# Kernel tuning notes

Measured on AMD Instinct MI355X. Metric: run time of the kernel, lower is better.

Reference implementation:

```python
import jax, jax.numpy as jnp
import numpy as np

N, D_PHY, D_BOND, VOC = 512, 4, 128, 1024


def setup_inputs() -> dict:
    rng = np.random.default_rng(0)

    def cplx(shape, scale=1.0):
        return ((rng.standard_normal(shape) + 1j * rng.standard_normal(shape)) * scale).astype(np.complex64)

    A = cplx((VOC, D_PHY, D_PHY))                      # raw embedding params (QR applied in forward, as in torch M property)
    B0 = cplx((D_PHY, 1, D_BOND), 1.0 / np.sqrt(D_BOND))
    Bm = cplx((N - 2, D_PHY * D_BOND, D_BOND))
    Bm = np.linalg.qr(Bm)[0].reshape(N - 2, D_PHY, D_BOND, D_BOND).astype(np.complex64)  # left-isometric, as set_left_param
    Bl = cplx((D_PHY * D_BOND, 1))
    Bl = np.linalg.qr(Bl)[0].reshape(D_PHY, D_BOND, 1).astype(np.complex64)
    tokens = rng.integers(0, VOC, size=(N,))
    return {
        'a_re': jnp.asarray(A.real), 'a_im': jnp.asarray(A.imag),
        'b0_re': jnp.asarray(B0.real), 'b0_im': jnp.asarray(B0.imag),
        'bm_re': jnp.asarray(Bm.real), 'bm_im': jnp.asarray(Bm.imag),
        'bl_re': jnp.asarray(Bl.real), 'bl_im': jnp.asarray(Bl.imag),
        'tokens': jnp.asarray(tokens, dtype=jnp.int32),
    }


def _site(S, B, Mi):
    # S: (l, l') running density-like state; B: (p, l, r); Mi: (p, q) measurement op.
    # Equivalent to contracting torch's zipped = einsum(conj(B)[p,l,r], M[p,q], B[q,l',r'] -> [l,r,r',l'])
    # with the running state, but fused to avoid the (l,r,r',l') intermediate.
    t = jnp.einsum('ab,qbc->qac', S, B)      # (q, l, r')
    t = jnp.einsum('pq,qac->pac', Mi, t)     # (p, l, r')
    return jnp.einsum('plr,plc->rc', B.conj(), t)  # (r, r')


def reference(a_re, a_im, b0_re, b0_im, bm_re, bm_im, bl_re, bl_im, tokens):
    A = a_re + 1j * a_im                                  # (v, d, d)
    d = A.shape[-1]
    Aq = jnp.linalg.qr(A.reshape(-1, d))[0].reshape(A.shape)
    M = jnp.einsum('vij,vik->vjk', Aq.conj(), Aq)         # (v, d, d) POVM-like ops
    Ms = M[tokens]                                        # (n, d, d)

    B0 = b0_re + 1j * b0_im                               # (d, 1, D)
    Bm = bm_re + 1j * bm_im                               # (n-2, d, D, D)
    Bl = bl_re + 1j * bl_im                               # (d, D, 1)

    S = jnp.ones((1, 1), dtype=A.dtype)
    S = _site(S, B0, Ms[0])                               # (D, D)

    def step(S, xs):
        B, Mi = xs
        return _site(S, B, Mi), None

    S, _ = jax.lax.scan(step, S, (Bm, Ms[1:-1]))
    S = _site(S, Bl, Ms[-1])                              # (1, 1)
    return S.reshape(-1)                                  # complex64, shape (1,), as torch out.view(-1)
```

## Files before the change

kernel.cpp:

```cpp
#include <hip/hip_runtime.h>
#include <hip/hip_bf16.h>


__device__ __forceinline__ float2 cfma(float2 a, float2 b, float2 acc) {
    acc.x = fmaf(a.x, b.x, fmaf(-a.y, b.y, acc.x));
    acc.y = fmaf(a.x, b.y, fmaf( a.y, b.x, acc.y));
    return acc;
}
__device__ __forceinline__ float2 cfmac(float2 a, float2 b, float2 acc) {
    acc.x = fmaf(a.x, b.x, fmaf( a.y, b.y, acc.x));
    acc.y = fmaf(a.x, b.y, fmaf(-a.y, b.x, acc.y));
    return acc;
}

__device__ __forceinline__ float2 ld_coh(const float2* p) {
    union { unsigned long long u; float2 f; } cv;
    cv.u = __hip_atomic_load((const unsigned long long*)p,
                             __ATOMIC_RELAXED, __HIP_MEMORY_SCOPE_AGENT);
    return cv.f;
}
__device__ __forceinline__ void st_coh(float2* p, float2 x) {
    union { unsigned long long u; float2 f; } cv;
    cv.f = x;
    __hip_atomic_store((unsigned long long*)p, cv.u,
                       __ATOMIC_RELAXED, __HIP_MEMORY_SCOPE_AGENT);
}

__device__ __forceinline__ double2 d2mul(double2 a, double2 b) {
    return make_double2(a.x*b.x - a.y*b.y, a.x*b.y + a.y*b.x);
}
__device__ __forceinline__ double2 d2conj(double2 a) { return make_double2(a.x, -a.y); }
__device__ __forceinline__ double2 d2add(double2 a, double2 b) {
    return make_double2(a.x + b.x, a.y + b.y);
}
__device__ __forceinline__ double2 d2sub(double2 a, double2 b) {
    return make_double2(a.x - b.x, a.y - b.y);
}

__device__ __forceinline__ void lds_barrier() {
    asm volatile("s_waitcnt lgkmcnt(0)" ::: "memory");
    __builtin_amdgcn_s_barrier();
    __builtin_amdgcn_sched_barrier(0);
}

__device__ void redN(double2* v, int n, double2 (*redm)[4]) {
    for (int off = 32; off; off >>= 1) {
        for (int d = 0; d < n; ++d) {
            v[d].x += __shfl_down(v[d].x, off, 64);
            v[d].y += __shfl_down(v[d].y, off, 64);
        }
    }
    const int wid = threadIdx.x >> 6, lane = threadIdx.x & 63;
    __syncthreads();
    if (lane == 0)
        for (int d = 0; d < n; ++d) redm[wid][d] = v[d];
    __syncthreads();
    for (int d = 0; d < n; ++d) {
        double2 s = make_double2(0.0, 0.0);
        for (int w = 0; w < 9; ++w) { s.x += redm[w][d].x; s.y += redm[w][d].y; }
        v[d] = s;
    }
}

__device__ __forceinline__ float2 m_entry(const float* __restrict__ a_re,
                                          const float* __restrict__ a_im,
                                          int v, int m, const float2* Wl)
{
    const int j = m >> 2, k = m & 3;
    float2 Arow[4][4];
    #pragma unroll
    for (int i = 0; i < 4; ++i) {
        float4 re = *(const float4*)(a_re + v*16 + i*4);
        float4 im = *(const float4*)(a_im + v*16 + i*4);
        Arow[i][0] = make_float2(re.x, im.x);
        Arow[i][1] = make_float2(re.y, im.y);
        Arow[i][2] = make_float2(re.z, im.z);
        Arow[i][3] = make_float2(re.w, im.w);
    }
    float2 acc = make_float2(0.f, 0.f);
    #pragma unroll
    for (int i = 0; i < 4; ++i) {
        float2 yj = make_float2(0.f, 0.f), yk = yj;
        #pragma unroll
        for (int q = 0; q < 4; ++q) {
            yj = cfma(Arow[i][q], Wl[q*4 + j], yj);
            yk = cfma(Arow[i][q], Wl[q*4 + k], yk);
        }
        acc = cfmac(yj, yk, acc);
    }
    return acc;
}

__global__ __launch_bounds__(512) void zero_cnt(unsigned int* __restrict__ cnt)
{
    cnt[threadIdx.x] = 0u;
}

#define NWG 128u
__device__ __forceinline__ bool site_barrier(unsigned int* addr,
                                             unsigned* nzw, int* live_lds, int tid)
{
    asm volatile("s_waitcnt lgkmcnt(0)" ::: "memory");
    if (tid < 128) asm volatile("s_waitcnt vmcnt(0)" ::: "memory");
    __builtin_amdgcn_s_barrier();
    __builtin_amdgcn_sched_barrier(0);
    if (tid == 0) {
        unsigned add = 1u | ((nzw[0] | nzw[1]) ? 0x10000u : 0u);
        __hip_atomic_fetch_add(addr, add, __ATOMIC_RELAXED, __HIP_MEMORY_SCOPE_AGENT);
        unsigned v;
        for (;;) {
            v = __hip_atomic_load(addr, __ATOMIC_RELAXED, __HIP_MEMORY_SCOPE_AGENT);
            if ((v & 0xffffu) >= NWG) break;
            __builtin_amdgcn_s_sleep(1);
        }
        *live_lds = (int)(v >> 16);
    }
    asm volatile("s_waitcnt lgkmcnt(0)" ::: "memory");
    __builtin_amdgcn_s_barrier();
    __builtin_amdgcn_sched_barrier(0);
    return *live_lds != 0;
}

__global__ __launch_bounds__(576, 3) void scan_kernel(
    const float* __restrict__ a_re,  const float* __restrict__ a_im,
    const float* __restrict__ b0_re, const float* __restrict__ b0_im,
    const float* __restrict__ bm_re, const float* __restrict__ bm_im,
    const float* __restrict__ bl_re, const float* __restrict__ bl_im,
    const int*  __restrict__ tokens,
    float2* SbufA, float2* SbufB,
    unsigned int* cnt, float* out, int out_size)
{
    const int tid = threadIdx.x;
    const int bid = blockIdx.x;
    const int c   = ((bid & 7) << 4) | (bid >> 3);
    const int i16 = bid >> 3;

    __shared__ float2 Clds[4][128];
    __shared__ float4 Upart4[8][256];
    __shared__ float4 U4[256];
    __shared__ float4 P16_4[16][64];
    __shared__ float2 Bpre[2][4][128];
    __shared__ float2 fred[16];
    __shared__ double2 redm[9][4];
    __shared__ float2 Wlds[16];
    __shared__ float2 MtLds[2][16];
    __shared__ unsigned nzw[2];
    __shared__ int live_lds;

    const int a = tid & 127;
    const int h = tid >> 7;

    float2* Sread = SbufA;
    float2* Swrite = SbufB;
    bool dead = false;
    float warmacc = 0.f;
    float wm0 = 0.f, wm1 = 0.f, wm2 = 0.f, wm3 = 0.f;

    if (tid < 512) {
        const float4* t0r = (const float4*)bm_re + i16*1024;
        const float4* t0i = (const float4*)bm_im + i16*1024;
        #pragma unroll
        for (int k = 0; k < 2; ++k) {
            float4 x0 = t0r[tid + k*512],          y0 = t0i[tid + k*512];
            float4 x1 = t0r[16384 + tid + k*512],  y1 = t0i[16384 + tid + k*512];
            warmacc += x0.x+x0.y+x0.z+x0.w + y0.x+y0.y+y0.z+y0.w
                     + x1.x+x1.y+x1.z+x1.w + y1.x+y1.y+y1.z+y1.w;
        }
    }

    double2 gp[10];
    #pragma unroll
    for (int e = 0; e < 10; ++e) gp[e] = make_double2(0.0, 0.0);
    if (tid < 512) {
        for (int rr = 0; rr < 8; ++rr) {
            const int r = tid * 8 + rr;
            float4 fre = *(const float4*)(a_re + r*4);
            float4 fim = *(const float4*)(a_im + r*4);
            double r0 = fre.x, r1 = fre.y, r2 = fre.z, r3 = fre.w;
            double i0 = fim.x, i1 = fim.y, i2 = fim.z, i3 = fim.w;
#define GACC(e, rj, ij, rk, ik) \
            gp[e].x += rj*rk + ij*ik; gp[e].y += rj*ik - ij*rk;
            GACC(0, r0, i0, r0, i0)  GACC(1, r0, i0, r1, i1)
            GACC(2, r0, i0, r2, i2)  GACC(3, r0, i0, r3, i3)
            GACC(4, r1, i1, r1, i1)  GACC(5, r1, i1, r2, i2)
            GACC(6, r1, i1, r3, i3)  GACC(7, r2, i2, r2, i2)
            GACC(8, r2, i2, r3, i3)  GACC(9, r3, i3, r3, i3)
#undef GACC
        }
    }
    redN(gp + 0, 4, redm);
    redN(gp + 4, 4, redm);
    redN(gp + 8, 2, redm);

    double2 G4[4][4];
    G4[0][0]=gp[0]; G4[0][1]=gp[1]; G4[0][2]=gp[2]; G4[0][3]=gp[3];
    G4[1][1]=gp[4]; G4[1][2]=gp[5]; G4[1][3]=gp[6];
    G4[2][2]=gp[7]; G4[2][3]=gp[8]; G4[3][3]=gp[9];
    G4[1][0]=d2conj(gp[1]); G4[2][0]=d2conj(gp[2]); G4[3][0]=d2conj(gp[3]);
    G4[2][1]=d2conj(gp[5]); G4[3][1]=d2conj(gp[6]); G4[3][2]=d2conj(gp[8]);
    G4[0][0].y=0.0; G4[1][1].y=0.0; G4[2][2].y=0.0; G4[3][3].y=0.0;

    {
        double2 T[4][4];
        #pragma unroll
        for (int i = 0; i < 4; ++i)
            #pragma unroll
            for (int j = 0; j < 4; ++j)
                T[i][j] = make_double2((double)a_re[i*4+j], (double)a_im[i*4+j]);

        double dsgn[4];
        #pragma unroll
        for (int k = 0; k < 4; ++k) {
            double ssum = 0.0;
            #pragma unroll
            for (int i = 0; i < 4; ++i)
                if (i <= k) ssum += T[i][k].x*T[i][k].x + T[i][k].y*T[i][k].y;
            double xn = G4[k][k].x - ssum; if (xn < 0.0) xn = 0.0;
            double ar = T[k][k].x, ai = T[k][k].y;
            double nrm = sqrt(ar*ar + ai*ai + xn);
            double beta = (ar >= 0.0) ? -nrm : nrm;
            dsgn[k] = (beta >= 0.0) ? 1.0 : -1.0;
            double2 tau = make_double2((beta - ar)/beta, -ai/beta);
            double dr = ar - beta, di = ai;
            double dd = dr*dr + di*di;
            double2 s = make_double2(dr/dd, -di/dd);
            double2 w[4];
            #pragma unroll
            for (int j = 0; j < 4; ++j) if (j > k) {
                double2 acc = G4[k][j];
                #pragma unroll
                for (int i = 0; i < 4; ++i)
                    if (i <= k) acc = d2sub(acc, d2mul(d2conj(T[i][k]), T[i][j]));
                w[j] = d2add(T[k][j], d2mul(d2conj(s), acc));
            }
            #pragma unroll
            for (int j = 0; j < 4; ++j) if (j > k) {
                double2 tw = d2mul(tau, w[j]);
                T[k][j] = d2sub(T[k][j], tw);
                #pragma unroll
                for (int i = 0; i < 4; ++i)
                    if (i > k) T[i][j] = d2sub(T[i][j], d2mul(tw, d2mul(s, T[i][k])));
            }
            T[k][k] = make_double2(beta, 0.0);
            #pragma unroll
            for (int i = 0; i < 4; ++i)
                if (i > k) T[i][k] = make_double2(0.0, 0.0);
        }

        double2 R[4][4];
        #pragma unroll
        for (int k = 0; k < 4; ++k) {
            double dk = G4[k][k].x;
            #pragma unroll
            for (int i = 0; i < 4; ++i)
                if (i < k) dk -= R[i][k].x*R[i][k].x + R[i][k].y*R[i][k].y;
            if (dk < 1e-30) dk = 1e-30;
            double rkk = sqrt(dk);
            R[k][k] = make_double2(rkk, 0.0);
            #pragma unroll
            for (int j = 0; j < 4; ++j) if (j > k) {
                double2 acc = G4[k][j];
                #pragma unroll
                for (int i = 0; i < 4; ++i)
                    if (i < k) acc = d2sub(acc, d2mul(d2conj(R[i][k]), R[i][j]));
                R[k][j] = make_double2(acc.x/rkk, acc.y/rkk);
            }
        }
        double2 X[4][4];
        #pragma unroll
        for (int j = 0; j < 4; ++j) {
            #pragma unroll
            for (int i = 0; i < 4; ++i) X[i][j] = make_double2(0.0, 0.0);
            X[j][j] = make_double2(1.0 / R[j][j].x, 0.0);
            #pragma unroll
            for (int ii = 0; ii < 3; ++ii) {
                const int i = j - 1 - ii;
                if (i >= 0) {
                    double2 acc = make_double2(0.0, 0.0);
                    #pragma unroll
                    for (int m2 = 0; m2 < 4; ++m2)
                        if (m2 > i && m2 <= j) acc = d2add(acc, d2mul(R[i][m2], X[m2][j]));
                    X[i][j] = make_double2(-acc.x / R[i][i].x, -acc.y / R[i][i].x);
                }
            }
        }
        if (tid == 0) {
            #pragma unroll
            for (int q = 0; q < 4; ++q)
                #pragma unroll
                for (int j = 0; j < 4; ++j)
                    Wlds[q*4 + j] = make_float2((float)(X[q][j].x * dsgn[j]),
                                                (float)(X[q][j].y * dsgn[j]));
        }
    }
    __syncthreads();

    if (tid < 32) {
        const int which = tid >> 4, m = tid & 15;
        MtLds[which][m] = m_entry(a_re, a_im, tokens[which], m, Wlds);
    }
    if (tid < 512) {
        Bpre[1][h][a] = make_float2(bm_re[(h*128 + a)*128 + c],
                                    bm_im[(h*128 + a)*128 + c]);
    }
    __syncthreads();

    if (tid < 128) {
        const int r = a;
        float2 brr[4], bcc[4];
        for (int p = 0; p < 4; ++p) {
            brr[p] = make_float2(b0_re[p*128 + r], b0_im[p*128 + r]);
            bcc[p] = make_float2(b0_re[p*128 + c], b0_im[p*128 + c]);
        }
        float2 acc = make_float2(0.f, 0.f);
        for (int p = 0; p < 4; ++p) {
            float2 tp = make_float2(0.f, 0.f);
            for (int q = 0; q < 4; ++q) tp = cfma(MtLds[0][p*4 + q], bcc[q], tp);
            acc = cfmac(brr[p], tp, acc);
        }
        st_coh(&SbufA[c*128 + r], acc);
        int nz = (acc.x != 0.f) || (acc.y != 0.f);
        unsigned long long m = __ballot(nz);
        if ((tid & 63) == 0) nzw[tid >> 6] = (m != 0ULL) ? 1u : 0u;
    }

    if (!site_barrier(&cnt[0], nzw, &live_lds, tid)) dead = true;

    if (!dead) {
        for (int t = 1; t <= 510; ++t) {
            const int cur = t & 1, nxt = cur ^ 1;
            const float* br = bm_re + (size_t)(t - 1) * 65536;
            const float* bi = bm_im + (size_t)(t - 1) * 65536;

            float2 bp[8];
            float2 macc = make_float2(0.f, 0.f);
            int j = 0;
            if (tid >= 512) {
                j = tid - 512;
                warmacc += wm0 + wm1 + wm2 + wm3;
                if (t < 510) {
                    const float* br2 = bm_re + (size_t)t * 65536;
                    const float* bi2 = bm_im + (size_t)t * 65536;
                    #pragma unroll
                    for (int e = 0; e < 8; ++e) {
                        const int idx = j + e*64, q = idx >> 7, a2i = idx & 127;
                        bp[e] = make_float2(br2[(q*128 + a2i)*128 + c],
                                            bi2[(q*128 + a2i)*128 + c]);
                    }
                }
                if (j < 16) macc = m_entry(a_re, a_im, tokens[t+1], j, Wlds);
                if (t < 509) {
                    const float* wr = bm_re + (size_t)(t+1)*65536 + i16*4096;
                    const float* wi = bm_im + (size_t)(t+1)*65536 + i16*4096;
                    wm0 = wr[j*32];  wm1 = wr[2048 + j*32];
                    wm2 = wi[j*32];  wm3 = wi[2048 + j*32];
                } else { wm0 = wm1 = wm2 = wm3 = 0.f; }
            }

            if (tid < 512) {
                float2 acc = make_float2(0.f, 0.f);
                #pragma unroll
                for (int q = 0; q < 4; ++q)
                    acc = cfma(MtLds[cur][h*4 + q], Bpre[cur][q][a], acc);
                Clds[h][a] = acc;
            }
            lds_barrier();

            if (tid < 512) {
                const int sub = tid >> 6, a2 = tid & 63;
                float2 u00 = make_float2(0,0), u01 = u00, u02 = u00, u03 = u00;
                float2 u10 = u00, u11 = u00, u12 = u00, u13 = u00;
                {
                    const float2* _b0 = Sread + (sub*16)*128 + 2*a2;
                    const float2* _b1 = _b0 + 512;
                    const float2* _b2 = _b0 + 1024;
                    const float2* _b3 = _b0 + 1536;
                    float4 t0,t1,t2,t3,t4,t5,t6,t7,t8,t9,t10,t11,t12,t13,t14,t15;
                    asm volatile(
                      "global_load_dwordx4 %0, %16, off sc0 sc1\n\t"
                      "global_load_dwordx4 %1, %16, off offset:1024 sc0 sc1\n\t"
                      "global_load_dwordx4 %2, %16, off offset:2048 sc0 sc1\n\t"
                      "global_load_dwordx4 %3, %16, off offset:3072 sc0 sc1\n\t"
                      "global_load_dwordx4 %4, %17, off sc0 sc1\n\t"
                      "global_load_dwordx4 %5, %17, off offset:1024 sc0 sc1\n\t"
                      "global_load_dwordx4 %6, %17, off offset:2048 sc0 sc1\n\t"
                      "global_load_dwordx4 %7, %17, off offset:3072 sc0 sc1\n\t"
                      "global_load_dwordx4 %8, %18, off sc0 sc1\n\t"
                      "global_load_dwordx4 %9, %18, off offset:1024 sc0 sc1\n\t"
                      "global_load_dwordx4 %10, %18, off offset:2048 sc0 sc1\n\t"
                      "global_load_dwordx4 %11, %18, off offset:3072 sc0 sc1\n\t"
                      "global_load_dwordx4 %12, %19, off sc0 sc1\n\t"
                      "global_load_dwordx4 %13, %19, off offset:1024 sc0 sc1\n\t"
                      "global_load_dwordx4 %14, %19, off offset:2048 sc0 sc1\n\t"
                      "global_load_dwordx4 %15, %19, off offset:3072 sc0 sc1\n\t"
                      "s_waitcnt vmcnt(0)"
                      : "=&v"(t0), "=&v"(t1), "=&v"(t2), "=&v"(t3),
                        "=&v"(t4), "=&v"(t5), "=&v"(t6), "=&v"(t7),
                        "=&v"(t8), "=&v"(t9), "=&v"(t10), "=&v"(t11),
                        "=&v"(t12), "=&v"(t13), "=&v"(t14), "=&v"(t15)
                      : "v"(_b0), "v"(_b1), "v"(_b2), "v"(_b3));
                    float4 tt[16] = {t0,t1,t2,t3,t4,t5,t6,t7,
                                     t8,t9,t10,t11,t12,t13,t14,t15};
                    #pragma unroll
                    for (int e = 0; e < 16; ++e) {
                        const int b = sub*16 + e;
                        float2 slo = make_float2(tt[e].x, tt[e].y);
                        float2 shi = make_float2(tt[e].z, tt[e].w);
                        float2 c0 = Clds[0][b], c1 = Clds[1][b];
                        float2 c2 = Clds[2][b], c3 = Clds[3][b];
                        u00 = cfma(slo, c0, u00);  u10 = cfma(shi, c0, u10);
                        u01 = cfma(slo, c1, u01);  u11 = cfma(shi, c1, u11);
                        u02 = cfma(slo, c2, u02);  u12 = cfma(shi, c2, u12);
                        u03 = cfma(slo, c3, u03);  u13 = cfma(shi, c3, u13);
                    }
                }
                Upart4[sub][0*64 + a2] = make_float4(u00.x,u00.y,u10.x,u10.y);
                Upart4[sub][1*64 + a2] = make_float4(u01.x,u01.y,u11.x,u11.y);
                Upart4[sub][2*64 + a2] = make_float4(u02.x,u02.y,u12.x,u12.y);
                Upart4[sub][3*64 + a2] = make_float4(u03.x,u03.y,u13.x,u13.y);
            }
            lds_barrier();
            if (tid < 256) {
                float4 s = Upart4[0][tid];
                #pragma unroll
                for (int w = 1; w < 8; ++w) {
                    float4 x = Upart4[w][tid];
                    s.x += x.x; s.y += x.y; s.z += x.z; s.w += x.w;
                }
                U4[tid] = s;
            }
            lds_barrier();

            if (tid < 512) {
                const int pg = tid >> 5, r4 = tid & 31;
                const int p = pg >> 2, abase = (pg & 3) * 32;
                const int pabase = pg * 32;
                const float4* br4 = (const float4*)br;
                const float4* bi4 = (const float4*)bi;
                float2 o0 = make_float2(0,0), o1 = o0, o2 = o0, o3 = o0;
                #pragma unroll 4
                for (int k = 0; k < 32; k += 2) {
                    float4 u2 = U4[p*64 + ((abase + k) >> 1)];
                    float2 Ua = make_float2(u2.x, u2.y);
                    float2 Ub = make_float2(u2.z, u2.w);
                    float4 ra = br4[(pabase + k)*32 + r4];
                    float4 ia = bi4[(pabase + k)*32 + r4];
                    float4 rb = br4[(pabase + k + 1)*32 + r4];
                    float4 ib = bi4[(pabase + k + 1)*32 + r4];
                    o0 = cfmac(make_float2(ra.x, ia.x), Ua, o0);
                    o1 = cfmac(make_float2(ra.y, ia.y), Ua, o1);
                    o2 = cfmac(make_float2(ra.z, ia.z), Ua, o2);
                    o3 = cfmac(make_float2(ra.w, ia.w), Ua, o3);
                    o0 = cfmac(make_float2(rb.x, ib.x), Ub, o0);
                    o1 = cfmac(make_float2(rb.y, ib.y), Ub, o1);
                    o2 = cfmac(make_float2(rb.z, ib.z), Ub, o2);
                    o3 = cfmac(make_float2(rb.w, ib.w), Ub, o3);
                }
                P16_4[pg][r4]      = make_float4(o0.x,o0.y,o1.x,o1.y);
                P16_4[pg][32 + r4] = make_float4(o2.x,o2.y,o3.x,o3.y);
            }
            lds_barrier();
            if (tid < 128) {
                const int r = a;
                const int m = r & 3, q = r >> 2;
                const int pidx = (m < 2) ? (2*q + m) : (64 + 2*q + (m - 2));
                const float2* Prow = (const float2*)(&P16_4[0][0]);
                float2 fin = make_float2(0,0);
                #pragma unroll
                for (int w = 0; w < 16; ++w) {
                    float2 x = Prow[w*128 + pidx];
                    fin.x += x.x; fin.y += x.y;
                }
                st_coh(&Swrite[c * 128 + r], fin);
                int nz = (fin.x != 0.f) || (fin.y != 0.f);
                unsigned long long m2 = __ballot(nz);
                if ((tid & 63) == 0) nzw[tid >> 6] = (m2 != 0ULL) ? 1u : 0u;
            }

            if (tid >= 512) {
                if (t < 510) {
                    #pragma unroll
                    for (int e = 0; e < 8; ++e) {
                        const int idx = j + e*64, q = idx >> 7, a2i = idx & 127;
                        Bpre[nxt][q][a2i] = bp[e];
                    }
                }
                if (j < 16) MtLds[nxt][j] = macc;
            }

            if (!site_barrier(&cnt[t], nzw, &live_lds, tid)) { dead = true; break; }
            float2* tmp = Sread; Sread = Swrite; Swrite = tmp;
        }
    }
    warmacc += wm0 + wm1 + wm2 + wm3;

    if (out_size < 0) out[2] = warmacc;

    if (dead) {
        if (bid == 0 && tid == 0) {
            out[0] = 0.f;
            if (out_size > 1) out[1] = 0.f;
        }
        return;
    }
    if (bid != 0) return;

    if (tid < 512) {
        float2 acc = make_float2(0,0);
        for (int b = 0; b < 128; ++b) {
            float2 s = ld_coh(&Sread[b * 128 + a]);
            float2 bl = make_float2(bl_re[h*128 + b], bl_im[h*128 + b]);
            acc = cfma(s, bl, acc);
        }
        Clds[h][a] = acc;
    }
    __syncthreads();
    float2 tot = make_float2(0,0);
    if (tid < 512) {
        float2 tp = make_float2(0,0);
        for (int q = 0; q < 4; ++q) tp = cfma(MtLds[1][h*4 + q], Clds[q][a], tp);
        float2 blv = make_float2(bl_re[h*128 + a], bl_im[h*128 + a]);
        tot = cfmac(blv, tp, make_float2(0,0));
    }
    for (int off = 32; off; off >>= 1) {
        tot.x += __shfl_down(tot.x, off, 64);
        tot.y += __shfl_down(tot.y, off, 64);
    }
    if ((tid & 63) == 0) fred[tid >> 6] = tot;
    __syncthreads();
    if (tid == 0) {
        float2 s = make_float2(0,0);
        for (int w = 0; w < 9; ++w) { s.x += fred[w].x; s.y += fred[w].y; }
        out[0] = s.x;
        if (out_size > 1) out[1] = s.y;
    }
}

extern "C" void kernel_launch(void* const* d_in, const int* in_sizes, int n_in,
                              void* d_out, int out_size, void* d_ws, size_t ws_size,
                              hipStream_t stream)
{
    const float* a_re  = (const float*)d_in[0];
    const float* a_im  = (const float*)d_in[1];
    const float* b0_re = (const float*)d_in[2];
    const float* b0_im = (const float*)d_in[3];
    const float* bm_re = (const float*)d_in[4];
    const float* bm_im = (const float*)d_in[5];
    const float* bl_re = (const float*)d_in[6];
    const float* bl_im = (const float*)d_in[7];
    const int*  tokens = (const int*)d_in[8];

    char* ws = (char*)d_ws;
    float2* S0   = (float2*)(ws + 196608);
    float2* S1b  = (float2*)(ws + 327680);
    unsigned int* cnt = (unsigned int*)(ws + 458752);

    zero_cnt<<<dim3(1), dim3(512), 0, stream>>>(cnt);

    float* outf = (float*)d_out;
    int osz = out_size;
    void* args[] = {
        (void*)&a_re, (void*)&a_im, (void*)&b0_re, (void*)&b0_im,
        (void*)&bm_re, (void*)&bm_im, (void*)&bl_re, (void*)&bl_im,
        (void*)&tokens,
        (void*)&S0, (void*)&S1b, (void*)&cnt, (void*)&outf, (void*)&osz
    };
    hipLaunchCooperativeKernel((const void*)scan_kernel, dim3(128), dim3(576),
                               args, 0, stream);
}
```

Baseline: 226.6 us.

## Move QR whitening prep into single-block prep kernel and double-buffer Clds per site

The Gram-matrix reduction and 4x4 QR/triangular-inverse that every one of the 128 cooperative blocks repeated at kernel start now run once in a small prep kernel that also zeroes the counters. The scan kernel just loads the 16-entry whitening matrix from global memory. Inside the site loop, the M·B contraction into Clds is now computed for the next site before the grid barrier and double-buffered, removing one intra-block LDS barrier from the critical path of each step. Launch bounds drop from 3 to 2 waves per EU, which gives more registers but may change occupancy, and the prep kernel adds a serialized launch.

New measurement: 206.7 us. 1.1x faster.

```diff
diff --git a/kernel.cpp b/kernel.cpp
--- a/kernel.cpp
+++ b/kernel.cpp
@@ -41,25 +41,6 @@
     asm volatile("s_waitcnt lgkmcnt(0)" ::: "memory");
     __builtin_amdgcn_s_barrier();
     __builtin_amdgcn_sched_barrier(0);
-}
-
-__device__ void redN(double2* v, int n, double2 (*redm)[4]) {
-    for (int off = 32; off; off >>= 1) {
-        for (int d = 0; d < n; ++d) {
-            v[d].x += __shfl_down(v[d].x, off, 64);
-            v[d].y += __shfl_down(v[d].y, off, 64);
-        }
-    }
-    const int wid = threadIdx.x >> 6, lane = threadIdx.x & 63;
-    __syncthreads();
-    if (lane == 0)
-        for (int d = 0; d < n; ++d) redm[wid][d] = v[d];
-    __syncthreads();
-    for (int d = 0; d < n; ++d) {
-        double2 s = make_double2(0.0, 0.0);
-        for (int w = 0; w < 9; ++w) { s.x += redm[w][d].x; s.y += redm[w][d].y; }
-        v[d] = s;
-    }
 }
 
 __device__ __forceinline__ float2 m_entry(const float* __restrict__ a_re,
@@ -91,9 +72,156 @@
     return acc;
 }
 
-__global__ __launch_bounds__(512) void zero_cnt(unsigned int* __restrict__ cnt)
+__device__ void redN10(double2* v, double2 (*redm)[10]) {
+    for (int off = 32; off; off >>= 1) {
+        #pragma unroll
+        for (int d = 0; d < 10; ++d) {
+            v[d].x += __shfl_down(v[d].x, off, 64);
+            v[d].y += __shfl_down(v[d].y, off, 64);
+        }
+    }
+    const int wid = threadIdx.x >> 6, lane = threadIdx.x & 63;
+    __syncthreads();
+    if (lane == 0)
+        #pragma unroll
+        for (int d = 0; d < 10; ++d) redm[wid][d] = v[d];
+    __syncthreads();
+    #pragma unroll
+    for (int d = 0; d < 10; ++d) {
+        double2 s = make_double2(0.0, 0.0);
+        for (int w = 0; w < 8; ++w) { s.x += redm[w][d].x; s.y += redm[w][d].y; }
+        v[d] = s;
+    }
+}
+
+__global__ __launch_bounds__(512) void prep_kernel(const float* __restrict__ a_re,
+                                                   const float* __restrict__ a_im,
+                                                   float2* __restrict__ Wout,
+                                                   unsigned int* __restrict__ cnt)
 {
-    cnt[threadIdx.x] = 0u;
+    const int t = threadIdx.x;
+    cnt[t] = 0u;
+    __shared__ double2 redm[8][10];
+
+    double2 gp[10];
+    #pragma unroll
+    for (int e = 0; e < 10; ++e) gp[e] = make_double2(0.0, 0.0);
+    for (int rr = 0; rr < 8; ++rr) {
+        const int r = t * 8 + rr;
+        float4 fre = *(const float4*)(a_re + r*4);
+        float4 fim = *(const float4*)(a_im + r*4);
+        double r0 = fre.x, r1 = fre.y, r2 = fre.z, r3 = fre.w;
+        double i0 = fim.x, i1 = fim.y, i2 = fim.z, i3 = fim.w;
+#define GACC(e, rj, ij, rk, ik) \
+        gp[e].x += rj*rk + ij*ik; gp[e].y += rj*ik - ij*rk;
+        GACC(0, r0, i0, r0, i0)  GACC(1, r0, i0, r1, i1)
+        GACC(2, r0, i0, r2, i2)  GACC(3, r0, i0, r3, i3)
+        GACC(4, r1, i1, r1, i1)  GACC(5, r1, i1, r2, i2)
+        GACC(6, r1, i1, r3, i3)  GACC(7, r2, i2, r2, i2)
+        GACC(8, r2, i2, r3, i3)  GACC(9, r3, i3, r3, i3)
+#undef GACC
+    }
+    redN10(gp, redm);
+
+    if (t != 0) return;
+
+    double2 G4[4][4];
+    G4[0][0]=gp[0]; G4[0][1]=gp[1]; G4[0][2]=gp[2]; G4[0][3]=gp[3];
+    G4[1][1]=gp[4]; G4[1][2]=gp[5]; G4[1][3]=gp[6];
+    G4[2][2]=gp[7]; G4[2][3]=gp[8]; G4[3][3]=gp[9];
+    G4[1][0]=d2conj(gp[1]); G4[2][0]=d2conj(gp[2]); G4[3][0]=d2conj(gp[3]);
+    G4[2][1]=d2conj(gp[5]); G4[3][1]=d2conj(gp[6]); G4[3][2]=d2conj(gp[8]);
+    G4[0][0].y=0.0; G4[1][1].y=0.0; G4[2][2].y=0.0; G4[3][3].y=0.0;
+
+    double2 T[4][4];
+    #pragma unroll
+    for (int i = 0; i < 4; ++i)
+        #pragma unroll
+        for (int j = 0; j < 4; ++j)
+            T[i][j] = make_double2((double)a_re[i*4+j], (double)a_im[i*4+j]);
+
+    double dsgn[4];
+    #pragma unroll
+    for (int k = 0; k < 4; ++k) {
+        double ssum = 0.0;
+        #pragma unroll
+        for (int i = 0; i < 4; ++i)
+            if (i <= k) ssum += T[i][k].x*T[i][k].x + T[i][k].y*T[i][k].y;
+        double xn = G4[k][k].x - ssum; if (xn < 0.0) xn = 0.0;
+        double ar = T[k][k].x, ai = T[k][k].y;
+        double nrm = sqrt(ar*ar + ai*ai + xn);
+        double beta = (ar >= 0.0) ? -nrm : nrm;
+        dsgn[k] = (beta >= 0.0) ? 1.0 : -1.0;
+        double2 tau = make_double2((beta - ar)/beta, -ai/beta);
+        double dr = ar - beta, di = ai;
+        double dd = dr*dr + di*di;
+        double2 s = make_double2(dr/dd, -di/dd);
+        double2 w[4];
+        #pragma unroll
+        for (int j = 0; j < 4; ++j) if (j > k) {
+            double2 acc = G4[k][j];
+            #pragma unroll
+            for (int i = 0; i < 4; ++i)
+                if (i <= k) acc = d2sub(acc, d2mul(d2conj(T[i][k]), T[i][j]));
+            w[j] = d2add(T[k][j], d2mul(d2conj(s), acc));
+        }
+        #pragma unroll
+        for (int j = 0; j < 4; ++j) if (j > k) {
+            double2 tw = d2mul(tau, w[j]);
+            T[k][j] = d2sub(T[k][j], tw);
+            #pragma unroll
+            for (int i = 0; i < 4; ++i)
+                if (i > k) T[i][j] = d2sub(T[i][j], d2mul(tw, d2mul(s, T[i][k])));
+        }
+        T[k][k] = make_double2(beta, 0.0);
+        #pragma unroll
+        for (int i = 0; i < 4; ++i)
+            if (i > k) T[i][k] = make_double2(0.0, 0.0);
+    }
+
+    double2 R[4][4];
+    #pragma unroll
+    for (int k = 0; k < 4; ++k) {
+        double dk = G4[k][k].x;
+        #pragma unroll
+        for (int i = 0; i < 4; ++i)
+            if (i < k) dk -= R[i][k].x*R[i][k].x + R[i][k].y*R[i][k].y;
+        if (dk < 1e-30) dk = 1e-30;
+        double rkk = sqrt(dk);
+        R[k][k] = make_double2(rkk, 0.0);
+        #pragma unroll
+        for (int j = 0; j < 4; ++j) if (j > k) {
+            double2 acc = G4[k][j];
+            #pragma unroll
+            for (int i = 0; i < 4; ++i)
+                if (i < k) acc = d2sub(acc, d2mul(d2conj(R[i][k]), R[i][j]));
+            R[k][j] = make_double2(acc.x/rkk, acc.y/rkk);
+        }
+    }
+    double2 X[4][4];
+    #pragma unroll
+    for (int j = 0; j < 4; ++j) {
+        #pragma unroll
+        for (int i = 0; i < 4; ++i) X[i][j] = make_double2(0.0, 0.0);
+        X[j][j] = make_double2(1.0 / R[j][j].x, 0.0);
+        #pragma unroll
+        for (int ii = 0; ii < 3; ++ii) {
+            const int i = j - 1 - ii;
+            if (i >= 0) {
+                double2 acc = make_double2(0.0, 0.0);
+                #pragma unroll
+                for (int m2 = 0; m2 < 4; ++m2)
+                    if (m2 > i && m2 <= j) acc = d2add(acc, d2mul(R[i][m2], X[m2][j]));
+                X[i][j] = make_double2(-acc.x / R[i][i].x, -acc.y / R[i][i].x);
+            }
+        }
+    }
+    #pragma unroll
+    for (int q = 0; q < 4; ++q)
+        #pragma unroll
+        for (int j = 0; j < 4; ++j)
+            Wout[q*4 + j] = make_float2((float)(X[q][j].x * dsgn[j]),
+                                        (float)(X[q][j].y * dsgn[j]));
 }
 
 #define NWG 128u
@@ -121,12 +249,12 @@
     return *live_lds != 0;
 }
 
-__global__ __launch_bounds__(576, 3) void scan_kernel(
+__global__ __launch_bounds__(576, 2) void scan_kernel(
     const float* __restrict__ a_re,  const float* __restrict__ a_im,
     const float* __restrict__ b0_re, const float* __restrict__ b0_im,
     const float* __restrict__ bm_re, const float* __restrict__ bm_im,
     const float* __restrict__ bl_re, const float* __restrict__ bl_im,
-    const int*  __restrict__ tokens,
+    const int*  __restrict__ tokens, const float2* __restrict__ Wglob,
     float2* SbufA, float2* SbufB,
     unsigned int* cnt, float* out, int out_size)
 {
@@ -135,13 +263,12 @@
     const int c   = ((bid & 7) << 4) | (bid >> 3);
     const int i16 = bid >> 3;
 
-    __shared__ float2 Clds[4][128];
+    __shared__ float2 Clds[2][4][128];
     __shared__ float4 Upart4[8][256];
     __shared__ float4 U4[256];
     __shared__ float4 P16_4[16][64];
     __shared__ float2 Bpre[2][4][128];
     __shared__ float2 fred[16];
-    __shared__ double2 redm[9][4];
     __shared__ float2 Wlds[16];
     __shared__ float2 MtLds[2][16];
     __shared__ unsigned nzw[2];
@@ -168,131 +295,7 @@
         }
     }
 
-    double2 gp[10];
-    #pragma unroll
-    for (int e = 0; e < 10; ++e) gp[e] = make_double2(0.0, 0.0);
-    if (tid < 512) {
-        for (int rr = 0; rr < 8; ++rr) {
-            const int r = tid * 8 + rr;
-            float4 fre = *(const float4*)(a_re + r*4);
-            float4 fim = *(const float4*)(a_im + r*4);
-            double r0 = fre.x, r1 = fre.y, r2 = fre.z, r3 = fre.w;
-            double i0 = fim.x, i1 = fim.y, i2 = fim.z, i3 = fim.w;
-#define GACC(e, rj, ij, rk, ik) \
-            gp[e].x += rj*rk + ij*ik; gp[e].y += rj*ik - ij*rk;
-            GACC(0, r0, i0, r0, i0)  GACC(1, r0, i0, r1, i1)
-            GACC(2, r0, i0, r2, i2)  GACC(3, r0, i0, r3, i3)
-            GACC(4, r1, i1, r1, i1)  GACC(5, r1, i1, r2, i2)
-            GACC(6, r1, i1, r3, i3)  GACC(7, r2, i2, r2, i2)
-            GACC(8, r2, i2, r3, i3)  GACC(9, r3, i3, r3, i3)
-#undef GACC
-        }
-    }
-    redN(gp + 0, 4, redm);
-    redN(gp + 4, 4, redm);
-    redN(gp + 8, 2, redm);
-
-    double2 G4[4][4];
-    G4[0][0]=gp[0]; G4[0][1]=gp[1]; G4[0][2]=gp[2]; G4[0][3]=gp[3];
-    G4[1][1]=gp[4]; G4[1][2]=gp[5]; G4[1][3]=gp[6];
-    G4[2][2]=gp[7]; G4[2][3]=gp[8]; G4[3][3]=gp[9];
-    G4[1][0]=d2conj(gp[1]); G4[2][0]=d2conj(gp[2]); G4[3][0]=d2conj(gp[3]);
-    G4[2][1]=d2conj(gp[5]); G4[3][1]=d2conj(gp[6]); G4[3][2]=d2conj(gp[8]);
-    G4[0][0].y=0.0; G4[1][1].y=0.0; G4[2][2].y=0.0; G4[3][3].y=0.0;
-
-    {
-        double2 T[4][4];
-        #pragma unroll
-        for (int i = 0; i < 4; ++i)
-            #pragma unroll
-            for (int j = 0; j < 4; ++j)
-                T[i][j] = make_double2((double)a_re[i*4+j], (double)a_im[i*4+j]);
-
-        double dsgn[4];
-        #pragma unroll
-        for (int k = 0; k < 4; ++k) {
-            double ssum = 0.0;
-            #pragma unroll
-            for (int i = 0; i < 4; ++i)
-                if (i <= k) ssum += T[i][k].x*T[i][k].x + T[i][k].y*T[i][k].y;
-            double xn = G4[k][k].x - ssum; if (xn < 0.0) xn = 0.0;
-            double ar = T[k][k].x, ai = T[k][k].y;
-            double nrm = sqrt(ar*ar + ai*ai + xn);
-            double beta = (ar >= 0.0) ? -nrm : nrm;
-            dsgn[k] = (beta >= 0.0) ? 1.0 : -1.0;
-            double2 tau = make_double2((beta - ar)/beta, -ai/beta);
-            double dr = ar - beta, di = ai;
-            double dd = dr*dr + di*di;
-            double2 s = make_double2(dr/dd, -di/dd);
-            double2 w[4];
-            #pragma unroll
-            for (int j = 0; j < 4; ++j) if (j > k) {
-                double2 acc = G4[k][j];
-                #pragma unroll
-                for (int i = 0; i < 4; ++i)
-                    if (i <= k) acc = d2sub(acc, d2mul(d2conj(T[i][k]), T[i][j]));
-                w[j] = d2add(T[k][j], d2mul(d2conj(s), acc));
-            }
-            #pragma unroll
-            for (int j = 0; j < 4; ++j) if (j > k) {
-                double2 tw = d2mul(tau, w[j]);
-                T[k][j] = d2sub(T[k][j], tw);
-                #pragma unroll
-                for (int i = 0; i < 4; ++i)
-                    if (i > k) T[i][j] = d2sub(T[i][j], d2mul(tw, d2mul(s, T[i][k])));
-            }
-            T[k][k] = make_double2(beta, 0.0);
-            #pragma unroll
-            for (int i = 0; i < 4; ++i)
-                if (i > k) T[i][k] = make_double2(0.0, 0.0);
-        }
-
-        double2 R[4][4];
-        #pragma unroll
-        for (int k = 0; k < 4; ++k) {
-            double dk = G4[k][k].x;
-            #pragma unroll
-            for (int i = 0; i < 4; ++i)
-                if (i < k) dk -= R[i][k].x*R[i][k].x + R[i][k].y*R[i][k].y;
-            if (dk < 1e-30) dk = 1e-30;
-            double rkk = sqrt(dk);
-            R[k][k] = make_double2(rkk, 0.0);
-            #pragma unroll
-            for (int j = 0; j < 4; ++j) if (j > k) {
-                double2 acc = G4[k][j];
-                #pragma unroll
-                for (int i = 0; i < 4; ++i)
-                    if (i < k) acc = d2sub(acc, d2mul(d2conj(R[i][k]), R[i][j]));
-                R[k][j] = make_double2(acc.x/rkk, acc.y/rkk);
-            }
-        }
-        double2 X[4][4];
-        #pragma unroll
-        for (int j = 0; j < 4; ++j) {
-            #pragma unroll
-            for (int i = 0; i < 4; ++i) X[i][j] = make_double2(0.0, 0.0);
-            X[j][j] = make_double2(1.0 / R[j][j].x, 0.0);
-            #pragma unroll
-            for (int ii = 0; ii < 3; ++ii) {
-                const int i = j - 1 - ii;
-                if (i >= 0) {
-                    double2 acc = make_double2(0.0, 0.0);
-                    #pragma unroll
-                    for (int m2 = 0; m2 < 4; ++m2)
-                        if (m2 > i && m2 <= j) acc = d2add(acc, d2mul(R[i][m2], X[m2][j]));
-                    X[i][j] = make_double2(-acc.x / R[i][i].x, -acc.y / R[i][i].x);
-                }
-            }
-        }
-        if (tid == 0) {
-            #pragma unroll
-            for (int q = 0; q < 4; ++q)
-                #pragma unroll
-                for (int j = 0; j < 4; ++j)
-                    Wlds[q*4 + j] = make_float2((float)(X[q][j].x * dsgn[j]),
-                                                (float)(X[q][j].y * dsgn[j]));
-        }
-    }
+    if (tid < 16) Wlds[tid] = Wglob[tid];
     __syncthreads();
 
     if (tid < 32) {
@@ -305,6 +308,13 @@
     }
     __syncthreads();
 
+    if (tid < 512) {
+        float2 acc = make_float2(0.f, 0.f);
+        #pragma unroll
+        for (int q = 0; q < 4; ++q)
+            acc = cfma(MtLds[1][h*4 + q], Bpre[1][q][a], acc);
+        Clds[1][h][a] = acc;
+    }
     if (tid < 128) {
         const int r = a;
         float2 brr[4], bcc[4];
@@ -358,16 +368,8 @@
             }
 
             if (tid < 512) {
-                float2 acc = make_float2(0.f, 0.f);
-                #pragma unroll
-                for (int q = 0; q < 4; ++q)
-                    acc = cfma(MtLds[cur][h*4 + q], Bpre[cur][q][a], acc);
-                Clds[h][a] = acc;
-            }
-            lds_barrier();
-
-            if (tid < 512) {
                 const int sub = tid >> 6, a2 = tid & 63;
+                const float2 (*CB)[128] = Clds[cur];
                 float2 u00 = make_float2(0,0), u01 = u00, u02 = u00, u03 = u00;
                 float2 u10 = u00, u11 = u00, u12 = u00, u13 = u00;
                 {
@@ -406,8 +408,8 @@
                         const int b = sub*16 + e;
                         float2 slo = make_float2(tt[e].x, tt[e].y);
                         float2 shi = make_float2(tt[e].z, tt[e].w);
-                        float2 c0 = Clds[0][b], c1 = Clds[1][b];
-                        float2 c2 = Clds[2][b], c3 = Clds[3][b];
+                        float2 c0 = CB[0][b], c1 = CB[1][b];
+                        float2 c2 = CB[2][b], c3 = CB[3][b];
                         u00 = cfma(slo, c0, u00);  u10 = cfma(shi, c0, u10);
                         u01 = cfma(slo, c1, u01);  u11 = cfma(shi, c1, u11);
                         u02 = cfma(slo, c2, u02);  u12 = cfma(shi, c2, u12);
@@ -487,6 +489,15 @@
                 }
                 if (j < 16) MtLds[nxt][j] = macc;
             }
+            lds_barrier();
+
+            if (t < 510 && tid < 512) {
+                float2 acc = make_float2(0.f, 0.f);
+                #pragma unroll
+                for (int q = 0; q < 4; ++q)
+                    acc = cfma(MtLds[nxt][h*4 + q], Bpre[nxt][q][a], acc);
+                Clds[nxt][h][a] = acc;
+            }
 
             if (!site_barrier(&cnt[t], nzw, &live_lds, tid)) { dead = true; break; }
             float2* tmp = Sread; Sread = Swrite; Swrite = tmp;
@@ -512,13 +523,13 @@
             float2 bl = make_float2(bl_re[h*128 + b], bl_im[h*128 + b]);
             acc = cfma(s, bl, acc);
         }
-        Clds[h][a] = acc;
+        Clds[0][h][a] = acc;
     }
     __syncthreads();
     float2 tot = make_float2(0,0);
     if (tid < 512) {
         float2 tp = make_float2(0,0);
-        for (int q = 0; q < 4; ++q) tp = cfma(MtLds[1][h*4 + q], Clds[q][a], tp);
+        for (int q = 0; q < 4; ++q) tp = cfma(MtLds[1][h*4 + q], Clds[0][q][a], tp);
         float2 blv = make_float2(bl_re[h*128 + a], bl_im[h*128 + a]);
         tot = cfmac(blv, tp, make_float2(0,0));
     }
@@ -554,15 +565,16 @@
     float2* S0   = (float2*)(ws + 196608);
     float2* S1b  = (float2*)(ws + 327680);
     unsigned int* cnt = (unsigned int*)(ws + 458752);
-
-    zero_cnt<<<dim3(1), dim3(512), 0, stream>>>(cnt);
+    float2* W    = (float2*)(ws + 460800);
+
+    prep_kernel<<<dim3(1), dim3(512), 0, stream>>>(a_re, a_im, W, cnt);
 
     float* outf = (float*)d_out;
     int osz = out_size;
     void* args[] = {
         (void*)&a_re, (void*)&a_im, (void*)&b0_re, (void*)&b0_im,
         (void*)&bm_re, (void*)&bm_im, (void*)&bl_re, (void*)&bl_im,
-        (void*)&tokens,
+        (void*)&tokens, (void*)&W,
         (void*)&S0, (void*)&S1b, (void*)&cnt, (void*)&outf, (void*)&osz
     };
     hipLaunchCooperativeKernel((const void*)scan_kernel, dim3(128), dim3(576),
```
